# Optimization experiments

Measured on AMD Instinct MI355X. Metric: run time of the kernel, lower is better.

Reference implementation:

```python
import jax, jax.numpy as jnp
import numpy as np

N = 50000   # nodes
E = 800000  # directed edges
IN, H1, H2, OUT = 128, 64, 32, 40
K = 2       # SGConv hops


def setup_inputs() -> dict:
    key = jax.random.key(0)
    ks = jax.random.split(key, 8)
    x = jax.random.normal(ks[0], (N, IN), dtype=jnp.float32)
    edge_index = jax.random.randint(ks[1], (2, E), 0, N, dtype=jnp.int64)
    s = lambda k, shp, fan: jax.random.normal(k, shp, dtype=jnp.float32) / np.sqrt(fan)
    return {
        "x": x,
        "edge_index": edge_index,
        "W1": s(ks[2], (IN, H1), IN), "b1": jnp.zeros((H1,), jnp.float32),
        "W2": s(ks[3], (H1, H2), H1), "b2": jnp.zeros((H2,), jnp.float32),
        "Wf": s(ks[4], (H2, OUT), H2), "bf": jnp.zeros((OUT,), jnp.float32),
    }


def _gcn_norm(edge_index, num_nodes):
    # add self-loops, then norm = d^{-1/2}[src] * d^{-1/2}[dst], d over targets
    loop = jnp.arange(num_nodes, dtype=edge_index.dtype)
    src = jnp.concatenate([edge_index[0], loop])
    dst = jnp.concatenate([edge_index[1], loop])
    deg = jax.ops.segment_sum(jnp.ones_like(src, dtype=jnp.float32), dst,
                              num_segments=num_nodes)
    dinv = jnp.where(deg > 0, jax.lax.rsqrt(deg), 0.0)
    norm = dinv[src] * dinv[dst]  # [E + N]
    return src, dst, norm


def _propagate_k(x, src, dst, norm, num_nodes, k):
    for _ in range(k):
        x = jax.ops.segment_sum(x[src] * norm[:, None], dst,
                                num_segments=num_nodes)
    return x


def reference(x, edge_index, W1, b1, W2, b2, Wf, bf):
    num_nodes = x.shape[0]
    src, dst, norm = _gcn_norm(edge_index, num_nodes)
    # SGConv layer 1: A_hat^K x, then linear, then relu
    h = _propagate_k(x, src, dst, norm, num_nodes, K)
    h = jax.nn.relu(h @ W1 + b1)
    # SGConv layer 2
    h = _propagate_k(h, src, dst, norm, num_nodes, K)
    h = jax.nn.relu(h @ W2 + b2)
    embedding = h
    logits = h @ Wf + bf
    return (embedding, logits)
```

## Files before the change

kernel.cpp:

```cpp
#include <hip/hip_runtime.h>

#define NN 50000
#define NE 800000
#define IN_F 128
#define H1_F 64
#define H2_F 32
#define OUT_F 40

#define BSH 7
#define NBKT 391
#define CAPA 4032
#define CHUNK 4096
#define NCH ((NE + CHUNK - 1) / CHUNK)

static inline int cdiv(int a, int b) { return (a + b - 1) / b; }

__global__ void initcur_k(int* __restrict__ gCursor) {
    int b = blockIdx.x * 256 + threadIdx.x;
    if (b < NBKT) gCursor[b] = b * CAPA;
}

__global__ __launch_bounds__(256)
void binA_k(const int* __restrict__ src, const int* __restrict__ dst,
            uint2* __restrict__ pairs, int* __restrict__ gCursor) {
    __shared__ int hist[512], incl[512], runSt[512], lcur[512], baseSh[512];
    __shared__ uint2 stage[CHUNK];
    const int t = threadIdx.x;
    const int e0 = blockIdx.x * CHUNK;
    const int n = min(CHUNK, NE - e0);

    hist[t] = 0; hist[t + 256] = 0;
    __syncthreads();
    for (int i = t; i < n; i += 256) {
        int d = dst[e0 + i];
        atomicAdd(&hist[d >> BSH], 1);
    }
    __syncthreads();
    incl[t] = hist[t]; incl[t + 256] = hist[t + 256];
    __syncthreads();
    for (int off = 1; off < 512; off <<= 1) {
        int v0 = (t >= off) ? incl[t - off] : 0;
        int v1 = (t + 256 >= off) ? incl[t + 256 - off] : 0;
        __syncthreads();
        incl[t] += v0; incl[t + 256] += v1;
        __syncthreads();
    }
    runSt[t] = incl[t] - hist[t];   runSt[t + 256] = incl[t + 256] - hist[t + 256];
    lcur[t]  = runSt[t];            lcur[t + 256]  = runSt[t + 256];
    __syncthreads();
    for (int i = t; i < n; i += 256) {
        int s = src[e0 + i], d = dst[e0 + i];
        int b = d >> BSH;
        int p = atomicAdd(&lcur[b], 1);
        stage[p] = make_uint2((unsigned)s, (unsigned)d);
    }
    for (int b = t; b < NBKT; b += 256) {
        int c = hist[b];
        baseSh[b] = c ? atomicAdd(&gCursor[b], c) : 0;
    }
    __syncthreads();
    for (int i = t; i < n; i += 256) {
        uint2 p = stage[i];
        int b = (int)(p.y >> BSH);
        int gp = baseSh[b] + (i - runSt[b]);
        if (gp < (b + 1) * CAPA) pairs[gp] = p;
    }
}

__global__ __launch_bounds__(512)
void segscan_k(const int* __restrict__ gCursor, int* __restrict__ segBase) {
    __shared__ int sh[512], orig[512];
    int t = threadIdx.x;
    int c = 0;
    if (t < NBKT) {
        c = gCursor[t] - t * CAPA;
        c = max(0, min(c, CAPA));
    }
    sh[t] = c; orig[t] = c;
    __syncthreads();
    for (int off = 1; off < 512; off <<= 1) {
        int v = (t >= off) ? sh[t - off] : 0;
        __syncthreads();
        sh[t] += v;
        __syncthreads();
    }
    if (t < NBKT) segBase[t] = sh[t] - orig[t];
}

__global__ __launch_bounds__(256)
void binB_k(const uint2* __restrict__ pairs, const int* __restrict__ gCursor,
            const int* __restrict__ segBase, int* __restrict__ cursor,
            float* __restrict__ dinv, int* __restrict__ csr) {
    const int b = blockIdx.x;
    const int nodeBase = b << BSH;
    const int nNodes = min(128, NN - nodeBase);
    int count = gCursor[b] - b * CAPA;
    count = max(0, min(count, CAPA));
    const int seg = segBase[b];
    __shared__ int hist[128], incl[128], lcur[128];
    const int t = threadIdx.x;
    if (t < 128) hist[t] = 0;
    __syncthreads();
    const uint2* bp = pairs + (size_t)b * CAPA;
    for (int i = t; i < count; i += 256) {
        int d = (int)bp[i].y - nodeBase;
        atomicAdd(&hist[d], 1);
    }
    __syncthreads();
    if (t < 128) incl[t] = hist[t];
    __syncthreads();
    for (int off = 1; off < 128; off <<= 1) {
        int v = (t < 128 && t >= off) ? incl[t - off] : 0;
        __syncthreads();
        if (t < 128) incl[t] += v;
        __syncthreads();
    }
    if (t < nNodes) {
        cursor[nodeBase + t] = seg + incl[t];
        dinv[nodeBase + t]   = rsqrtf((float)hist[t] + 1.0f);
        lcur[t] = seg + incl[t] - hist[t];
    }
    __syncthreads();
    for (int i = t; i < count; i += 256) {
        uint2 p = bp[i];
        int d = (int)p.y - nodeBase;
        int pos = atomicAdd(&lcur[d], 1);
        csr[pos] = (int)p.x;
    }
}

template<int K, int F, int CT, int RPT, int BLOCK, bool BIAS, bool SCALE>
__global__ __launch_bounds__(BLOCK)
void gemm_tile_k(const float* __restrict__ X, const float* __restrict__ W,
                 const float* __restrict__ b, const float* __restrict__ dinv,
                 float* __restrict__ Y) {
    constexpr int RT = BLOCK / CT;
    constexpr int TR = RT * RPT;
    constexpr int KT = 32;
    constexpr int KPAD = KT + 1;
    __shared__ float Xs[TR][KPAD];
    __shared__ float Wsh[KT][F];
    const int rowBase = blockIdx.x * TR;
    const int tc = threadIdx.x % CT;
    const int tr = threadIdx.x / CT;

    float acc[RPT][4];
    #pragma unroll
    for (int i = 0; i < RPT; ++i)
        #pragma unroll
        for (int j = 0; j < 4; ++j) acc[i][j] = 0.0f;

    for (int k0 = 0; k0 < K; k0 += KT) {
        constexpr int XL4 = TR * KT / 4;
        for (int l = threadIdx.x; l < XL4; l += BLOCK) {
            int r  = l / (KT / 4);
            int kk = (l % (KT / 4)) * 4;
            float4 v = make_float4(0.f, 0.f, 0.f, 0.f);
            int gr = rowBase + r;
            if (gr < NN) v = *reinterpret_cast<const float4*>(X + (size_t)gr * K + k0 + kk);
            Xs[r][kk + 0] = v.x; Xs[r][kk + 1] = v.y;
            Xs[r][kk + 2] = v.z; Xs[r][kk + 3] = v.w;
        }
        constexpr int WL4 = KT * F / 4;
        for (int l = threadIdx.x; l < WL4; l += BLOCK) {
            int kk = l / (F / 4);
            int c  = (l % (F / 4)) * 4;
            *reinterpret_cast<float4*>(&Wsh[kk][c]) =
                *reinterpret_cast<const float4*>(W + (size_t)(k0 + kk) * F + c);
        }
        __syncthreads();
        #pragma unroll
        for (int kk = 0; kk < KT; ++kk) {
            float wv[4];
            *reinterpret_cast<float4*>(wv) = *reinterpret_cast<const float4*>(&Wsh[kk][tc * 4]);
            #pragma unroll
            for (int i = 0; i < RPT; ++i) {
                float a = Xs[tr * RPT + i][kk];
                acc[i][0] = fmaf(a, wv[0], acc[i][0]);
                acc[i][1] = fmaf(a, wv[1], acc[i][1]);
                acc[i][2] = fmaf(a, wv[2], acc[i][2]);
                acc[i][3] = fmaf(a, wv[3], acc[i][3]);
            }
        }
        __syncthreads();
    }
    #pragma unroll
    for (int i = 0; i < RPT; ++i) {
        int gr = rowBase + tr * RPT + i;
        if (gr < NN) {
            float sc = SCALE ? dinv[gr] : 1.0f;
            float4 v;
            v.x = acc[i][0]; v.y = acc[i][1]; v.z = acc[i][2]; v.w = acc[i][3];
            if (BIAS) {
                v.x += b[tc * 4 + 0]; v.y += b[tc * 4 + 1];
                v.z += b[tc * 4 + 2]; v.w += b[tc * 4 + 3];
            }
            v.x *= sc; v.y *= sc; v.z *= sc; v.w *= sc;
            *reinterpret_cast<float4*>(Y + (size_t)gr * F + tc * 4) = v;
        }
    }
}

template<int F>
__global__ __launch_bounds__(256)
void pull4_k(const float* __restrict__ in, const int* __restrict__ csr,
             const int* __restrict__ cursor, const float* __restrict__ dinv,
             float* __restrict__ out) {
    constexpr int LPN = F / 4;
    constexpr int NPB = 256 / LPN;
    const int t = threadIdx.x;
    const int node = blockIdx.x * NPB + t / LPN;
    const int col  = (t % LPN) * 4;
    if (node >= NN) return;
    const int beg = (node == 0) ? 0 : cursor[node - 1];
    const int end = cursor[node];
    float4 a0 = *reinterpret_cast<const float4*>(in + (size_t)node * F + col);
    float4 a1 = make_float4(0.f, 0.f, 0.f, 0.f);
    float4 a2 = make_float4(0.f, 0.f, 0.f, 0.f);
    float4 a3 = make_float4(0.f, 0.f, 0.f, 0.f);
    int k = beg;
    for (; k + 3 < end; k += 4) {
        int s0 = csr[k], s1 = csr[k + 1], s2 = csr[k + 2], s3 = csr[k + 3];
        float4 v0 = *reinterpret_cast<const float4*>(in + (size_t)s0 * F + col);
        float4 v1 = *reinterpret_cast<const float4*>(in + (size_t)s1 * F + col);
        float4 v2 = *reinterpret_cast<const float4*>(in + (size_t)s2 * F + col);
        float4 v3 = *reinterpret_cast<const float4*>(in + (size_t)s3 * F + col);
        a0.x += v0.x; a0.y += v0.y; a0.z += v0.z; a0.w += v0.w;
        a1.x += v1.x; a1.y += v1.y; a1.z += v1.z; a1.w += v1.w;
        a2.x += v2.x; a2.y += v2.y; a2.z += v2.z; a2.w += v2.w;
        a3.x += v3.x; a3.y += v3.y; a3.z += v3.z; a3.w += v3.w;
    }
    for (; k < end; ++k) {
        int s0 = csr[k];
        float4 v0 = *reinterpret_cast<const float4*>(in + (size_t)s0 * F + col);
        a0.x += v0.x; a0.y += v0.y; a0.z += v0.z; a0.w += v0.w;
    }
    float sc = dinv[node]; sc *= sc;
    float4 r;
    r.x = (a0.x + a1.x + a2.x + a3.x) * sc;
    r.y = (a0.y + a1.y + a2.y + a3.y) * sc;
    r.z = (a0.z + a1.z + a2.z + a3.z) * sc;
    r.w = (a0.w + a1.w + a2.w + a3.w) * sc;
    *reinterpret_cast<float4*>(out + (size_t)node * F + col) = r;
}

__global__ __launch_bounds__(256)
void pullgemm2_k(const float* __restrict__ in, const int* __restrict__ csr,
                 const int* __restrict__ cursor, const float* __restrict__ dinv,
                 const float* __restrict__ b1, const float* __restrict__ W2,
                 float* __restrict__ outT) {
    __shared__ float hs[64][68];
    __shared__ float W2s[64][32];
    const int t = threadIdx.x;
    for (int i = t; i < 64 * 32 / 4; i += 256)
        reinterpret_cast<float4*>(&W2s[0][0])[i] = reinterpret_cast<const float4*>(W2)[i];
    const int nodeBase = blockIdx.x * 64;
    #pragma unroll
    for (int pass = 0; pass < 4; ++pass) {
        const int nb = pass * 16 + t / 16;
        const int node = nodeBase + nb;
        const int col = (t % 16) * 4;
        float4 r = make_float4(0.f, 0.f, 0.f, 0.f);
        if (node < NN) {
            const int beg = (node == 0) ? 0 : cursor[node - 1];
            const int end = cursor[node];
            float4 a0 = *reinterpret_cast<const float4*>(in + (size_t)node * 64 + col);
            float4 a1 = make_float4(0.f, 0.f, 0.f, 0.f);
            float4 a2 = make_float4(0.f, 0.f, 0.f, 0.f);
            float4 a3 = make_float4(0.f, 0.f, 0.f, 0.f);
            int k = beg;
            for (; k + 3 < end; k += 4) {
                int s0 = csr[k], s1 = csr[k + 1], s2 = csr[k + 2], s3 = csr[k + 3];
                float4 v0 = *reinterpret_cast<const float4*>(in + (size_t)s0 * 64 + col);
                float4 v1 = *reinterpret_cast<const float4*>(in + (size_t)s1 * 64 + col);
                float4 v2 = *reinterpret_cast<const float4*>(in + (size_t)s2 * 64 + col);
                float4 v3 = *reinterpret_cast<const float4*>(in + (size_t)s3 * 64 + col);
                a0.x += v0.x; a0.y += v0.y; a0.z += v0.z; a0.w += v0.w;
                a1.x += v1.x; a1.y += v1.y; a1.z += v1.z; a1.w += v1.w;
                a2.x += v2.x; a2.y += v2.y; a2.z += v2.z; a2.w += v2.w;
                a3.x += v3.x; a3.y += v3.y; a3.z += v3.z; a3.w += v3.w;
            }
            for (; k < end; ++k) {
                int s0 = csr[k];
                float4 v0 = *reinterpret_cast<const float4*>(in + (size_t)s0 * 64 + col);
                a0.x += v0.x; a0.y += v0.y; a0.z += v0.z; a0.w += v0.w;
            }
            const float sc = dinv[node];
            const float4 bv = *reinterpret_cast<const float4*>(b1 + col);
            r.x = fmaxf((a0.x + a1.x + a2.x + a3.x) * sc + bv.x, 0.f);
            r.y = fmaxf((a0.y + a1.y + a2.y + a3.y) * sc + bv.y, 0.f);
            r.z = fmaxf((a0.z + a1.z + a2.z + a3.z) * sc + bv.z, 0.f);
            r.w = fmaxf((a0.w + a1.w + a2.w + a3.w) * sc + bv.w, 0.f);
        }
        *reinterpret_cast<float4*>(&hs[nb][col]) = r;
    }
    __syncthreads();
    const int r = t / 4;
    const int c0 = (t % 4) * 8;
    float acc[8];
    #pragma unroll
    for (int j = 0; j < 8; ++j) acc[j] = 0.f;
    #pragma unroll 4
    for (int k = 0; k < 64; k += 4) {
        float4 av = *reinterpret_cast<const float4*>(&hs[r][k]);
        #pragma unroll
        for (int kk = 0; kk < 4; ++kk) {
            float a = (&av.x)[kk];
            float4 w0 = *reinterpret_cast<const float4*>(&W2s[k + kk][c0]);
            float4 w1 = *reinterpret_cast<const float4*>(&W2s[k + kk][c0 + 4]);
            acc[0] = fmaf(a, w0.x, acc[0]); acc[1] = fmaf(a, w0.y, acc[1]);
            acc[2] = fmaf(a, w0.z, acc[2]); acc[3] = fmaf(a, w0.w, acc[3]);
            acc[4] = fmaf(a, w1.x, acc[4]); acc[5] = fmaf(a, w1.y, acc[5]);
            acc[6] = fmaf(a, w1.z, acc[6]); acc[7] = fmaf(a, w1.w, acc[7]);
        }
    }
    const int node = nodeBase + r;
    if (node < NN) {
        const float sc = dinv[node];
        float4 o0, o1;
        o0.x = acc[0] * sc; o0.y = acc[1] * sc; o0.z = acc[2] * sc; o0.w = acc[3] * sc;
        o1.x = acc[4] * sc; o1.y = acc[5] * sc; o1.z = acc[6] * sc; o1.w = acc[7] * sc;
        *reinterpret_cast<float4*>(outT + (size_t)node * 32 + c0)     = o0;
        *reinterpret_cast<float4*>(outT + (size_t)node * 32 + c0 + 4) = o1;
    }
}

__global__ __launch_bounds__(256)
void pullgemmF_k(const float* __restrict__ in, const int* __restrict__ csr,
                 const int* __restrict__ cursor, const float* __restrict__ dinv,
                 const float* __restrict__ b2, const float* __restrict__ Wf,
                 const float* __restrict__ bf, float* __restrict__ embOut,
                 float* __restrict__ logits) {
    __shared__ float es[64][36];
    __shared__ float Wfs[32][40];
    __shared__ float bfs[40];
    const int t = threadIdx.x;
    for (int i = t; i < 32 * 40 / 4; i += 256)
        reinterpret_cast<float4*>(&Wfs[0][0])[i] = reinterpret_cast<const float4*>(Wf)[i];
    if (t < 40) bfs[t] = bf[t];
    const int nodeBase = blockIdx.x * 64;
    #pragma unroll
    for (int pass = 0; pass < 2; ++pass) {
        const int nb = pass * 32 + t / 8;
        const int node = nodeBase + nb;
        const int col = (t % 8) * 4;
        float4 r = make_float4(0.f, 0.f, 0.f, 0.f);
        if (node < NN) {
            const int beg = (node == 0) ? 0 : cursor[node - 1];
            const int end = cursor[node];
            float4 a0 = *reinterpret_cast<const float4*>(in + (size_t)node * 32 + col);
            float4 a1 = make_float4(0.f, 0.f, 0.f, 0.f);
            float4 a2 = make_float4(0.f, 0.f, 0.f, 0.f);
            float4 a3 = make_float4(0.f, 0.f, 0.f, 0.f);
            int k = beg;
            for (; k + 3 < end; k += 4) {
                int s0 = csr[k], s1 = csr[k + 1], s2 = csr[k + 2], s3 = csr[k + 3];
                float4 v0 = *reinterpret_cast<const float4*>(in + (size_t)s0 * 32 + col);
                float4 v1 = *reinterpret_cast<const float4*>(in + (size_t)s1 * 32 + col);
                float4 v2 = *reinterpret_cast<const float4*>(in + (size_t)s2 * 32 + col);
                float4 v3 = *reinterpret_cast<const float4*>(in + (size_t)s3 * 32 + col);
                a0.x += v0.x; a0.y += v0.y; a0.z += v0.z; a0.w += v0.w;
                a1.x += v1.x; a1.y += v1.y; a1.z += v1.z; a1.w += v1.w;
                a2.x += v2.x; a2.y += v2.y; a2.z += v2.z; a2.w += v2.w;
                a3.x += v3.x; a3.y += v3.y; a3.z += v3.z; a3.w += v3.w;
            }
            for (; k < end; ++k) {
                int s0 = csr[k];
                float4 v0 = *reinterpret_cast<const float4*>(in + (size_t)s0 * 32 + col);
                a0.x += v0.x; a0.y += v0.y; a0.z += v0.z; a0.w += v0.w;
            }
            const float sc = dinv[node];
            const float4 bv = *reinterpret_cast<const float4*>(b2 + col);
            r.x = fmaxf((a0.x + a1.x + a2.x + a3.x) * sc + bv.x, 0.f);
            r.y = fmaxf((a0.y + a1.y + a2.y + a3.y) * sc + bv.y, 0.f);
            r.z = fmaxf((a0.z + a1.z + a2.z + a3.z) * sc + bv.z, 0.f);
            r.w = fmaxf((a0.w + a1.w + a2.w + a3.w) * sc + bv.w, 0.f);
            *reinterpret_cast<float4*>(embOut + (size_t)node * 32 + col) = r;
        }
        *reinterpret_cast<float4*>(&es[nb][col]) = r;
    }
    __syncthreads();
    const int r = t / 4;
    const int c0 = (t % 4) * 10;
    float acc[10];
    #pragma unroll
    for (int j = 0; j < 10; ++j) acc[j] = bfs[c0 + j];
    #pragma unroll 4
    for (int k = 0; k < 32; k += 4) {
        float4 av = *reinterpret_cast<const float4*>(&es[r][k]);
        #pragma unroll
        for (int kk = 0; kk < 4; ++kk) {
            float a = (&av.x)[kk];
            #pragma unroll
            for (int j = 0; j < 10; ++j)
                acc[j] = fmaf(a, Wfs[k + kk][c0 + j], acc[j]);
        }
    }
    const int node = nodeBase + r;
    if (node < NN) {
        float* lp = logits + (size_t)node * 40 + c0;
        #pragma unroll
        for (int j = 0; j < 10; j += 2) {
            float2 o; o.x = acc[j]; o.y = acc[j + 1];
            *reinterpret_cast<float2*>(lp + j) = o;
        }
    }
}

extern "C" void kernel_launch(void* const* d_in, const int* in_sizes, int n_in,
                              void* d_out, int out_size, void* d_ws, size_t ws_size,
                              hipStream_t stream) {
    const float* x  = (const float*)d_in[0];
    const int*   ei = (const int*)d_in[1];
    const float* W1 = (const float*)d_in[2];
    const float* b1 = (const float*)d_in[3];
    const float* W2 = (const float*)d_in[4];
    const float* b2 = (const float*)d_in[5];
    const float* Wf = (const float*)d_in[6];
    const float* bf = (const float*)d_in[7];

    float* out    = (float*)d_out;
    float* embOut = out;
    float* logits = out + (size_t)NN * H2_F;

    const int* src = ei;
    const int* dst = ei + NE;

    float* ws       = (float*)d_ws;
    float* dinv     = ws;
    int*   cursor   = (int*)(ws + NN);
    int*   csr      = cursor + NN;
    int*   gCursor  = csr + NE;
    int*   segBase  = gCursor + 512;
    float* bufA     = (float*)(segBase + 512);
    float* bufB     = bufA + (size_t)NN * 64;
    uint2* pairs    = (uint2*)bufB;

    initcur_k<<<cdiv(NBKT, 256), 256, 0, stream>>>(gCursor);
    binA_k<<<NCH, 256, 0, stream>>>(src, dst, pairs, gCursor);
    segscan_k<<<1, 512, 0, stream>>>(gCursor, segBase);
    binB_k<<<NBKT, 256, 0, stream>>>(pairs, gCursor, segBase, cursor, dinv, csr);

    gemm_tile_k<IN_F, H1_F, 16, 4, 256, false, true>
        <<<cdiv(NN, 64), 256, 0, stream>>>(x, W1, nullptr, dinv, bufA);
    pull4_k<H1_F>
        <<<cdiv(NN, 256 / (H1_F / 4)), 256, 0, stream>>>(bufA, csr, cursor, dinv, bufB);
    pullgemm2_k
        <<<cdiv(NN, 64), 256, 0, stream>>>(bufB, csr, cursor, dinv, b1, W2, bufA);

    pull4_k<H2_F>
        <<<cdiv(NN, 256 / (H2_F / 4)), 256, 0, stream>>>(bufA, csr, cursor, dinv, bufB);
    pullgemmF_k
        <<<cdiv(NN, 64), 256, 0, stream>>>(bufB, csr, cursor, dinv, b2, Wf, bf, embOut, logits);
}
```

Measured before the change: 240.4 us.

## Overlap X·W1 GEMM with edge binning in one kernel; pack edges, drop segscan

Merges the first dense GEMM (x·W1) and the edge-binning pass into one launch using block-index specialisation with a shared LDS union, so the GEMM no longer waits on dinv. The dinv scaling moves into the first pull kernel, which now weights each neighbour by dinv[src]. Edges are packed into 32-bit words instead of uint2, and the CSR uses fixed per-bucket segments with an int2 rowptr, which removes the segscan kernel and the init kernel (replaced by a memset). This cuts launches and binning traffic, but adds an extra dinv gather per edge in the first propagation and assumes source ids fit in 16 bits.

```diff
diff --git a/kernel.cpp b/kernel.cpp
--- a/kernel.cpp
+++ b/kernel.cpp
@@ -12,99 +12,137 @@
 #define CAPA 4032
 #define CHUNK 4096
 #define NCH ((NE + CHUNK - 1) / CHUNK)
+#define NGEMM ((NN + 63) / 64)
 
 static inline int cdiv(int a, int b) { return (a + b - 1) / b; }
 
-__global__ void initcur_k(int* __restrict__ gCursor) {
-    int b = blockIdx.x * 256 + threadIdx.x;
-    if (b < NBKT) gCursor[b] = b * CAPA;
-}
-
-__global__ __launch_bounds__(256)
-void binA_k(const int* __restrict__ src, const int* __restrict__ dst,
-            uint2* __restrict__ pairs, int* __restrict__ gCursor) {
-    __shared__ int hist[512], incl[512], runSt[512], lcur[512], baseSh[512];
-    __shared__ uint2 stage[CHUNK];
-    const int t = threadIdx.x;
-    const int e0 = blockIdx.x * CHUNK;
-    const int n = min(CHUNK, NE - e0);
-
-    hist[t] = 0; hist[t + 256] = 0;
-    __syncthreads();
-    for (int i = t; i < n; i += 256) {
-        int d = dst[e0 + i];
-        atomicAdd(&hist[d >> BSH], 1);
-    }
-    __syncthreads();
-    incl[t] = hist[t]; incl[t + 256] = hist[t + 256];
-    __syncthreads();
-    for (int off = 1; off < 512; off <<= 1) {
-        int v0 = (t >= off) ? incl[t - off] : 0;
-        int v1 = (t + 256 >= off) ? incl[t + 256 - off] : 0;
-        __syncthreads();
-        incl[t] += v0; incl[t + 256] += v1;
-        __syncthreads();
-    }
-    runSt[t] = incl[t] - hist[t];   runSt[t + 256] = incl[t + 256] - hist[t + 256];
-    lcur[t]  = runSt[t];            lcur[t + 256]  = runSt[t + 256];
-    __syncthreads();
-    for (int i = t; i < n; i += 256) {
-        int s = src[e0 + i], d = dst[e0 + i];
-        int b = d >> BSH;
-        int p = atomicAdd(&lcur[b], 1);
-        stage[p] = make_uint2((unsigned)s, (unsigned)d);
-    }
-    for (int b = t; b < NBKT; b += 256) {
-        int c = hist[b];
-        baseSh[b] = c ? atomicAdd(&gCursor[b], c) : 0;
-    }
-    __syncthreads();
-    for (int i = t; i < n; i += 256) {
-        uint2 p = stage[i];
-        int b = (int)(p.y >> BSH);
-        int gp = baseSh[b] + (i - runSt[b]);
-        if (gp < (b + 1) * CAPA) pairs[gp] = p;
-    }
-}
-
-__global__ __launch_bounds__(512)
-void segscan_k(const int* __restrict__ gCursor, int* __restrict__ segBase) {
-    __shared__ int sh[512], orig[512];
-    int t = threadIdx.x;
-    int c = 0;
-    if (t < NBKT) {
-        c = gCursor[t] - t * CAPA;
-        c = max(0, min(c, CAPA));
-    }
-    sh[t] = c; orig[t] = c;
-    __syncthreads();
-    for (int off = 1; off < 512; off <<= 1) {
-        int v = (t >= off) ? sh[t - off] : 0;
-        __syncthreads();
-        sh[t] += v;
-        __syncthreads();
-    }
-    if (t < NBKT) segBase[t] = sh[t] - orig[t];
-}
-
-__global__ __launch_bounds__(256)
-void binB_k(const uint2* __restrict__ pairs, const int* __restrict__ gCursor,
-            const int* __restrict__ segBase, int* __restrict__ cursor,
-            float* __restrict__ dinv, int* __restrict__ csr) {
+__device__ __forceinline__ unsigned pack_e(int s, int d) {
+    return ((unsigned)(d >> BSH) << 23) | ((unsigned)s << 7) | (unsigned)(d & 127);
+}
+
+struct GemmLDS { float Xs[64][33]; float Wsh[32][64]; };
+struct BinALDS { int hist[512]; int incl[512]; int runSt[512]; int lcur[512]; int baseSh[512];
+                 unsigned stage[CHUNK]; };
+
+__global__ __launch_bounds__(256)
+void phase1_k(const float* __restrict__ x, const float* __restrict__ W1,
+              const int* __restrict__ src, const int* __restrict__ dst,
+              unsigned* __restrict__ pairs, int* __restrict__ gCursor,
+              float* __restrict__ t_out) {
+    __shared__ union { GemmLDS g; BinALDS a; } lds;
+    const int t = threadIdx.x;
+
+    if (blockIdx.x < NGEMM) {
+        const int rowBase = blockIdx.x * 64;
+        const int tc = t % 16;
+        const int tr = t / 16;
+        float acc[4][4];
+        #pragma unroll
+        for (int i = 0; i < 4; ++i)
+            #pragma unroll
+            for (int j = 0; j < 4; ++j) acc[i][j] = 0.0f;
+
+        for (int k0 = 0; k0 < IN_F; k0 += 32) {
+            for (int l = t; l < 64 * 8; l += 256) {
+                int r  = l / 8;
+                int kk = (l % 8) * 4;
+                float4 v = make_float4(0.f, 0.f, 0.f, 0.f);
+                int gr = rowBase + r;
+                if (gr < NN) v = *reinterpret_cast<const float4*>(x + (size_t)gr * IN_F + k0 + kk);
+                lds.g.Xs[r][kk + 0] = v.x; lds.g.Xs[r][kk + 1] = v.y;
+                lds.g.Xs[r][kk + 2] = v.z; lds.g.Xs[r][kk + 3] = v.w;
+            }
+            for (int l = t; l < 32 * 16; l += 256) {
+                int kk = l / 16;
+                int c  = (l % 16) * 4;
+                *reinterpret_cast<float4*>(&lds.g.Wsh[kk][c]) =
+                    *reinterpret_cast<const float4*>(W1 + (size_t)(k0 + kk) * H1_F + c);
+            }
+            __syncthreads();
+            #pragma unroll
+            for (int kk = 0; kk < 32; ++kk) {
+                float wv[4];
+                *reinterpret_cast<float4*>(wv) =
+                    *reinterpret_cast<const float4*>(&lds.g.Wsh[kk][tc * 4]);
+                #pragma unroll
+                for (int i = 0; i < 4; ++i) {
+                    float a = lds.g.Xs[tr * 4 + i][kk];
+                    acc[i][0] = fmaf(a, wv[0], acc[i][0]);
+                    acc[i][1] = fmaf(a, wv[1], acc[i][1]);
+                    acc[i][2] = fmaf(a, wv[2], acc[i][2]);
+                    acc[i][3] = fmaf(a, wv[3], acc[i][3]);
+                }
+            }
+            __syncthreads();
+        }
+        #pragma unroll
+        for (int i = 0; i < 4; ++i) {
+            int gr = rowBase + tr * 4 + i;
+            if (gr < NN) {
+                float4 v;
+                v.x = acc[i][0]; v.y = acc[i][1]; v.z = acc[i][2]; v.w = acc[i][3];
+                *reinterpret_cast<float4*>(t_out + (size_t)gr * H1_F + tc * 4) = v;
+            }
+        }
+    } else {
+        const int e0 = (blockIdx.x - NGEMM) * CHUNK;
+        const int n = min(CHUNK, NE - e0);
+        lds.a.hist[t] = 0; lds.a.hist[t + 256] = 0;
+        __syncthreads();
+        for (int i = t; i < n; i += 256) {
+            int d = dst[e0 + i];
+            atomicAdd(&lds.a.hist[d >> BSH], 1);
+        }
+        __syncthreads();
+        lds.a.incl[t] = lds.a.hist[t]; lds.a.incl[t + 256] = lds.a.hist[t + 256];
+        __syncthreads();
+        for (int off = 1; off < 512; off <<= 1) {
+            int v0 = (t >= off) ? lds.a.incl[t - off] : 0;
+            int v1 = (t + 256 >= off) ? lds.a.incl[t + 256 - off] : 0;
+            __syncthreads();
+            lds.a.incl[t] += v0; lds.a.incl[t + 256] += v1;
+            __syncthreads();
+        }
+        lds.a.runSt[t]       = lds.a.incl[t] - lds.a.hist[t];
+        lds.a.runSt[t + 256] = lds.a.incl[t + 256] - lds.a.hist[t + 256];
+        lds.a.lcur[t]        = lds.a.runSt[t];
+        lds.a.lcur[t + 256]  = lds.a.runSt[t + 256];
+        __syncthreads();
+        for (int i = t; i < n; i += 256) {
+            int s = src[e0 + i], d = dst[e0 + i];
+            int b = d >> BSH;
+            int p = atomicAdd(&lds.a.lcur[b], 1);
+            lds.a.stage[p] = pack_e(s, d);
+        }
+        for (int b = t; b < NBKT; b += 256) {
+            int c = lds.a.hist[b];
+            lds.a.baseSh[b] = c ? atomicAdd(&gCursor[b], c) : 0;
+        }
+        __syncthreads();
+        for (int i = t; i < n; i += 256) {
+            unsigned p = lds.a.stage[i];
+            int b = (int)(p >> 23);
+            int gp = lds.a.baseSh[b] + (i - lds.a.runSt[b]);
+            if (gp < CAPA) pairs[(size_t)b * CAPA + gp] = p;
+        }
+    }
+}
+
+__global__ __launch_bounds__(256)
+void binB_k(const unsigned* __restrict__ pairs, const int* __restrict__ gCursor,
+            int2* __restrict__ rowptr, float* __restrict__ dinv, int* __restrict__ csr) {
     const int b = blockIdx.x;
     const int nodeBase = b << BSH;
     const int nNodes = min(128, NN - nodeBase);
-    int count = gCursor[b] - b * CAPA;
-    count = max(0, min(count, CAPA));
-    const int seg = segBase[b];
+    int count = min(gCursor[b], CAPA);
+    const int seg = b * CAPA;
     __shared__ int hist[128], incl[128], lcur[128];
     const int t = threadIdx.x;
     if (t < 128) hist[t] = 0;
     __syncthreads();
-    const uint2* bp = pairs + (size_t)b * CAPA;
+    const unsigned* bp = pairs + (size_t)b * CAPA;
     for (int i = t; i < count; i += 256) {
-        int d = (int)bp[i].y - nodeBase;
-        atomicAdd(&hist[d], 1);
+        atomicAdd(&hist[bp[i] & 127], 1);
     }
     __syncthreads();
     if (t < 128) incl[t] = hist[t];
@@ -116,123 +154,96 @@
         __syncthreads();
     }
     if (t < nNodes) {
-        cursor[nodeBase + t] = seg + incl[t];
+        int e = seg + incl[t];
+        rowptr[nodeBase + t] = make_int2(e - hist[t], e);
         dinv[nodeBase + t]   = rsqrtf((float)hist[t] + 1.0f);
-        lcur[t] = seg + incl[t] - hist[t];
+        lcur[t] = e - hist[t];
     }
     __syncthreads();
     for (int i = t; i < count; i += 256) {
-        uint2 p = bp[i];
-        int d = (int)p.y - nodeBase;
-        int pos = atomicAdd(&lcur[d], 1);
-        csr[pos] = (int)p.x;
-    }
-}
-
-template<int K, int F, int CT, int RPT, int BLOCK, bool BIAS, bool SCALE>
-__global__ __launch_bounds__(BLOCK)
-void gemm_tile_k(const float* __restrict__ X, const float* __restrict__ W,
-                 const float* __restrict__ b, const float* __restrict__ dinv,
-                 float* __restrict__ Y) {
-    constexpr int RT = BLOCK / CT;
-    constexpr int TR = RT * RPT;
-    constexpr int KT = 32;
-    constexpr int KPAD = KT + 1;
-    __shared__ float Xs[TR][KPAD];
-    __shared__ float Wsh[KT][F];
-    const int rowBase = blockIdx.x * TR;
-    const int tc = threadIdx.x % CT;
-    const int tr = threadIdx.x / CT;
-
-    float acc[RPT][4];
-    #pragma unroll
-    for (int i = 0; i < RPT; ++i)
-        #pragma unroll
-        for (int j = 0; j < 4; ++j) acc[i][j] = 0.0f;
-
-    for (int k0 = 0; k0 < K; k0 += KT) {
-        constexpr int XL4 = TR * KT / 4;
-        for (int l = threadIdx.x; l < XL4; l += BLOCK) {
-            int r  = l / (KT / 4);
-            int kk = (l % (KT / 4)) * 4;
-            float4 v = make_float4(0.f, 0.f, 0.f, 0.f);
-            int gr = rowBase + r;
-            if (gr < NN) v = *reinterpret_cast<const float4*>(X + (size_t)gr * K + k0 + kk);
-            Xs[r][kk + 0] = v.x; Xs[r][kk + 1] = v.y;
-            Xs[r][kk + 2] = v.z; Xs[r][kk + 3] = v.w;
-        }
-        constexpr int WL4 = KT * F / 4;
-        for (int l = threadIdx.x; l < WL4; l += BLOCK) {
-            int kk = l / (F / 4);
-            int c  = (l % (F / 4)) * 4;
-            *reinterpret_cast<float4*>(&Wsh[kk][c]) =
-                *reinterpret_cast<const float4*>(W + (size_t)(k0 + kk) * F + c);
-        }
-        __syncthreads();
-        #pragma unroll
-        for (int kk = 0; kk < KT; ++kk) {
-            float wv[4];
-            *reinterpret_cast<float4*>(wv) = *reinterpret_cast<const float4*>(&Wsh[kk][tc * 4]);
-            #pragma unroll
-            for (int i = 0; i < RPT; ++i) {
-                float a = Xs[tr * RPT + i][kk];
-                acc[i][0] = fmaf(a, wv[0], acc[i][0]);
-                acc[i][1] = fmaf(a, wv[1], acc[i][1]);
-                acc[i][2] = fmaf(a, wv[2], acc[i][2]);
-                acc[i][3] = fmaf(a, wv[3], acc[i][3]);
-            }
-        }
-        __syncthreads();
-    }
-    #pragma unroll
-    for (int i = 0; i < RPT; ++i) {
-        int gr = rowBase + tr * RPT + i;
-        if (gr < NN) {
-            float sc = SCALE ? dinv[gr] : 1.0f;
-            float4 v;
-            v.x = acc[i][0]; v.y = acc[i][1]; v.z = acc[i][2]; v.w = acc[i][3];
-            if (BIAS) {
-                v.x += b[tc * 4 + 0]; v.y += b[tc * 4 + 1];
-                v.z += b[tc * 4 + 2]; v.w += b[tc * 4 + 3];
-            }
-            v.x *= sc; v.y *= sc; v.z *= sc; v.w *= sc;
-            *reinterpret_cast<float4*>(Y + (size_t)gr * F + tc * 4) = v;
-        }
-    }
-}
-
-template<int F>
-__global__ __launch_bounds__(256)
-void pull4_k(const float* __restrict__ in, const int* __restrict__ csr,
-             const int* __restrict__ cursor, const float* __restrict__ dinv,
+        unsigned p = bp[i];
+        int pos = atomicAdd(&lcur[p & 127], 1);
+        csr[pos] = (int)((p >> 7) & 0xFFFFu);
+    }
+}
+
+__global__ __launch_bounds__(256)
+void pull1_k(const float* __restrict__ in, const int* __restrict__ csr,
+             const int2* __restrict__ rowptr, const float* __restrict__ dinv,
              float* __restrict__ out) {
-    constexpr int LPN = F / 4;
-    constexpr int NPB = 256 / LPN;
-    const int t = threadIdx.x;
-    const int node = blockIdx.x * NPB + t / LPN;
-    const int col  = (t % LPN) * 4;
+    const int t = threadIdx.x;
+    const int node = blockIdx.x * 16 + t / 16;
+    const int col  = (t % 16) * 4;
     if (node >= NN) return;
-    const int beg = (node == 0) ? 0 : cursor[node - 1];
-    const int end = cursor[node];
-    float4 a0 = *reinterpret_cast<const float4*>(in + (size_t)node * F + col);
+    const int2 rp = rowptr[node];
+    const float dd = dinv[node];
+    float4 s4 = *reinterpret_cast<const float4*>(in + (size_t)node * 64 + col);
+    float4 a0, a1, a2, a3;
+    a0.x = dd * s4.x; a0.y = dd * s4.y; a0.z = dd * s4.z; a0.w = dd * s4.w;
+    a1 = make_float4(0.f, 0.f, 0.f, 0.f);
+    a2 = make_float4(0.f, 0.f, 0.f, 0.f);
+    a3 = make_float4(0.f, 0.f, 0.f, 0.f);
+    int k = rp.x;
+    for (; k + 3 < rp.y; k += 4) {
+        int s0 = csr[k], s1 = csr[k + 1], s2 = csr[k + 2], s3 = csr[k + 3];
+        float w0 = dinv[s0], w1 = dinv[s1], w2 = dinv[s2], w3 = dinv[s3];
+        float4 v0 = *reinterpret_cast<const float4*>(in + (size_t)s0 * 64 + col);
+        float4 v1 = *reinterpret_cast<const float4*>(in + (size_t)s1 * 64 + col);
+        float4 v2 = *reinterpret_cast<const float4*>(in + (size_t)s2 * 64 + col);
+        float4 v3 = *reinterpret_cast<const float4*>(in + (size_t)s3 * 64 + col);
+        a0.x = fmaf(w0, v0.x, a0.x); a0.y = fmaf(w0, v0.y, a0.y);
+        a0.z = fmaf(w0, v0.z, a0.z); a0.w = fmaf(w0, v0.w, a0.w);
+        a1.x = fmaf(w1, v1.x, a1.x); a1.y = fmaf(w1, v1.y, a1.y);
+        a1.z = fmaf(w1, v1.z, a1.z); a1.w = fmaf(w1, v1.w, a1.w);
+        a2.x = fmaf(w2, v2.x, a2.x); a2.y = fmaf(w2, v2.y, a2.y);
+        a2.z = fmaf(w2, v2.z, a2.z); a2.w = fmaf(w2, v2.w, a2.w);
+        a3.x = fmaf(w3, v3.x, a3.x); a3.y = fmaf(w3, v3.y, a3.y);
+        a3.z = fmaf(w3, v3.z, a3.z); a3.w = fmaf(w3, v3.w, a3.w);
+    }
+    for (; k < rp.y; ++k) {
+        int s0 = csr[k];
+        float w0 = dinv[s0];
+        float4 v0 = *reinterpret_cast<const float4*>(in + (size_t)s0 * 64 + col);
+        a0.x = fmaf(w0, v0.x, a0.x); a0.y = fmaf(w0, v0.y, a0.y);
+        a0.z = fmaf(w0, v0.z, a0.z); a0.w = fmaf(w0, v0.w, a0.w);
+    }
+    const float sc = dd * dd;
+    float4 r;
+    r.x = (a0.x + a1.x + a2.x + a3.x) * sc;
+    r.y = (a0.y + a1.y + a2.y + a3.y) * sc;
+    r.z = (a0.z + a1.z + a2.z + a3.z) * sc;
+    r.w = (a0.w + a1.w + a2.w + a3.w) * sc;
+    *reinterpret_cast<float4*>(out + (size_t)node * 64 + col) = r;
+}
+
+__global__ __launch_bounds__(256)
+void pull32_k(const float* __restrict__ in, const int* __restrict__ csr,
+              const int2* __restrict__ rowptr, const float* __restrict__ dinv,
+              float* __restrict__ out) {
+    const int t = threadIdx.x;
+    const int node = blockIdx.x * 32 + t / 8;
+    const int col  = (t % 8) * 4;
+    if (node >= NN) return;
+    const int2 rp = rowptr[node];
+    float4 a0 = *reinterpret_cast<const float4*>(in + (size_t)node * 32 + col);
     float4 a1 = make_float4(0.f, 0.f, 0.f, 0.f);
     float4 a2 = make_float4(0.f, 0.f, 0.f, 0.f);
     float4 a3 = make_float4(0.f, 0.f, 0.f, 0.f);
-    int k = beg;
-    for (; k + 3 < end; k += 4) {
+    int k = rp.x;
+    for (; k + 3 < rp.y; k += 4) {
         int s0 = csr[k], s1 = csr[k + 1], s2 = csr[k + 2], s3 = csr[k + 3];
-        float4 v0 = *reinterpret_cast<const float4*>(in + (size_t)s0 * F + col);
-        float4 v1 = *reinterpret_cast<const float4*>(in + (size_t)s1 * F + col);
-        float4 v2 = *reinterpret_cast<const float4*>(in + (size_t)s2 * F + col);
-        float4 v3 = *reinterpret_cast<const float4*>(in + (size_t)s3 * F + col);
+        float4 v0 = *reinterpret_cast<const float4*>(in + (size_t)s0 * 32 + col);
+        float4 v1 = *reinterpret_cast<const float4*>(in + (size_t)s1 * 32 + col);
+        float4 v2 = *reinterpret_cast<const float4*>(in + (size_t)s2 * 32 + col);
+        float4 v3 = *reinterpret_cast<const float4*>(in + (size_t)s3 * 32 + col);
         a0.x += v0.x; a0.y += v0.y; a0.z += v0.z; a0.w += v0.w;
         a1.x += v1.x; a1.y += v1.y; a1.z += v1.z; a1.w += v1.w;
         a2.x += v2.x; a2.y += v2.y; a2.z += v2.z; a2.w += v2.w;
         a3.x += v3.x; a3.y += v3.y; a3.z += v3.z; a3.w += v3.w;
     }
-    for (; k < end; ++k) {
+    for (; k < rp.y; ++k) {
         int s0 = csr[k];
-        float4 v0 = *reinterpret_cast<const float4*>(in + (size_t)s0 * F + col);
+        float4 v0 = *reinterpret_cast<const float4*>(in + (size_t)s0 * 32 + col);
         a0.x += v0.x; a0.y += v0.y; a0.z += v0.z; a0.w += v0.w;
     }
     float sc = dinv[node]; sc *= sc;
@@ -241,12 +252,12 @@
     r.y = (a0.y + a1.y + a2.y + a3.y) * sc;
     r.z = (a0.z + a1.z + a2.z + a3.z) * sc;
     r.w = (a0.w + a1.w + a2.w + a3.w) * sc;
-    *reinterpret_cast<float4*>(out + (size_t)node * F + col) = r;
+    *reinterpret_cast<float4*>(out + (size_t)node * 32 + col) = r;
 }
 
 __global__ __launch_bounds__(256)
 void pullgemm2_k(const float* __restrict__ in, const int* __restrict__ csr,
-                 const int* __restrict__ cursor, const float* __restrict__ dinv,
+                 const int2* __restrict__ rowptr, const float* __restrict__ dinv,
                  const float* __restrict__ b1, const float* __restrict__ W2,
                  float* __restrict__ outT) {
     __shared__ float hs[64][68];
@@ -262,14 +273,13 @@
         const int col = (t % 16) * 4;
         float4 r = make_float4(0.f, 0.f, 0.f, 0.f);
         if (node < NN) {
-            const int beg = (node == 0) ? 0 : cursor[node - 1];
-            const int end = cursor[node];
+            const int2 rp = rowptr[node];
             float4 a0 = *reinterpret_cast<const float4*>(in + (size_t)node * 64 + col);
             float4 a1 = make_float4(0.f, 0.f, 0.f, 0.f);
             float4 a2 = make_float4(0.f, 0.f, 0.f, 0.f);
             float4 a3 = make_float4(0.f, 0.f, 0.f, 0.f);
-            int k = beg;
-            for (; k + 3 < end; k += 4) {
+            int k = rp.x;
+            for (; k + 3 < rp.y; k += 4) {
                 int s0 = csr[k], s1 = csr[k + 1], s2 = csr[k + 2], s3 = csr[k + 3];
                 float4 v0 = *reinterpret_cast<const float4*>(in + (size_t)s0 * 64 + col);
                 float4 v1 = *reinterpret_cast<const float4*>(in + (size_t)s1 * 64 + col);
@@ -280,7 +290,7 @@
                 a2.x += v2.x; a2.y += v2.y; a2.z += v2.z; a2.w += v2.w;
                 a3.x += v3.x; a3.y += v3.y; a3.z += v3.z; a3.w += v3.w;
             }
-            for (; k < end; ++k) {
+            for (; k < rp.y; ++k) {
                 int s0 = csr[k];
                 float4 v0 = *reinterpret_cast<const float4*>(in + (size_t)s0 * 64 + col);
                 a0.x += v0.x; a0.y += v0.y; a0.z += v0.z; a0.w += v0.w;
@@ -327,7 +337,7 @@
 
 __global__ __launch_bounds__(256)
 void pullgemmF_k(const float* __restrict__ in, const int* __restrict__ csr,
-                 const int* __restrict__ cursor, const float* __restrict__ dinv,
+                 const int2* __restrict__ rowptr, const float* __restrict__ dinv,
                  const float* __restrict__ b2, const float* __restrict__ Wf,
                  const float* __restrict__ bf, float* __restrict__ embOut,
                  float* __restrict__ logits) {
@@ -346,14 +356,13 @@
         const int col = (t % 8) * 4;
         float4 r = make_float4(0.f, 0.f, 0.f, 0.f);
         if (node < NN) {
-            const int beg = (node == 0) ? 0 : cursor[node - 1];
-            const int end = cursor[node];
+            const int2 rp = rowptr[node];
             float4 a0 = *reinterpret_cast<const float4*>(in + (size_t)node * 32 + col);
             float4 a1 = make_float4(0.f, 0.f, 0.f, 0.f);
             float4 a2 = make_float4(0.f, 0.f, 0.f, 0.f);
             float4 a3 = make_float4(0.f, 0.f, 0.f, 0.f);
-            int k = beg;
-            for (; k + 3 < end; k += 4) {
+            int k = rp.x;
+            for (; k + 3 < rp.y; k += 4) {
                 int s0 = csr[k], s1 = csr[k + 1], s2 = csr[k + 2], s3 = csr[k + 3];
                 float4 v0 = *reinterpret_cast<const float4*>(in + (size_t)s0 * 32 + col);
                 float4 v1 = *reinterpret_cast<const float4*>(in + (size_t)s1 * 32 + col);
@@ -364,7 +373,7 @@
                 a2.x += v2.x; a2.y += v2.y; a2.z += v2.z; a2.w += v2.w;
                 a3.x += v3.x; a3.y += v3.y; a3.z += v3.z; a3.w += v3.w;
             }
-            for (; k < end; ++k) {
+            for (; k < rp.y; ++k) {
                 int s0 = csr[k];
                 float4 v0 = *reinterpret_cast<const float4*>(in + (size_t)s0 * 32 + col);
                 a0.x += v0.x; a0.y += v0.y; a0.z += v0.z; a0.w += v0.w;
@@ -426,30 +435,22 @@
     const int* src = ei;
     const int* dst = ei + NE;
 
-    float* ws       = (float*)d_ws;
-    float* dinv     = ws;
-    int*   cursor   = (int*)(ws + NN);
-    int*   csr      = cursor + NN;
-    int*   gCursor  = csr + NE;
-    int*   segBase  = gCursor + 512;
-    float* bufA     = (float*)(segBase + 512);
-    float* bufB     = bufA + (size_t)NN * 64;
-    uint2* pairs    = (uint2*)bufB;
-
-    initcur_k<<<cdiv(NBKT, 256), 256, 0, stream>>>(gCursor);
-    binA_k<<<NCH, 256, 0, stream>>>(src, dst, pairs, gCursor);
-    segscan_k<<<1, 512, 0, stream>>>(gCursor, segBase);
-    binB_k<<<NBKT, 256, 0, stream>>>(pairs, gCursor, segBase, cursor, dinv, csr);
-
-    gemm_tile_k<IN_F, H1_F, 16, 4, 256, false, true>
-        <<<cdiv(NN, 64), 256, 0, stream>>>(x, W1, nullptr, dinv, bufA);
-    pull4_k<H1_F>
-        <<<cdiv(NN, 256 / (H1_F / 4)), 256, 0, stream>>>(bufA, csr, cursor, dinv, bufB);
-    pullgemm2_k
-        <<<cdiv(NN, 64), 256, 0, stream>>>(bufB, csr, cursor, dinv, b1, W2, bufA);
-
-    pull4_k<H2_F>
-        <<<cdiv(NN, 256 / (H2_F / 4)), 256, 0, stream>>>(bufA, csr, cursor, dinv, bufB);
-    pullgemmF_k
-        <<<cdiv(NN, 64), 256, 0, stream>>>(bufB, csr, cursor, dinv, b2, Wf, bf, embOut, logits);
-}
+    float* ws      = (float*)d_ws;
+    float*    dinv   = ws;
+    int2*     rowptr = (int2*)(ws + NN);
+    int*      csr    = (int*)(rowptr + NN);
+    int*      gCursor= csr + (size_t)NBKT * CAPA;
+    float*    bufA   = (float*)(gCursor + 512);
+    float*    bufB   = bufA + (size_t)NN * 64;
+    unsigned* pairs  = (unsigned*)bufB;
+
+    hipMemsetAsync(gCursor, 0, NBKT * sizeof(int), stream);
+    phase1_k<<<NGEMM + NCH, 256, 0, stream>>>(x, W1, src, dst, pairs, gCursor, bufA);
+    binB_k<<<NBKT, 256, 0, stream>>>(pairs, gCursor, rowptr, dinv, csr);
+
+    pull1_k<<<cdiv(NN, 16), 256, 0, stream>>>(bufA, csr, rowptr, dinv, bufB);
+    pullgemm2_k<<<cdiv(NN, 64), 256, 0, stream>>>(bufB, csr, rowptr, dinv, b1, W2, bufA);
+
+    pull32_k<<<cdiv(NN, 32), 256, 0, stream>>>(bufA, csr, rowptr, dinv, bufB);
+    pullgemmF_k<<<cdiv(NN, 64), 256, 0, stream>>>(bufB, csr, rowptr, dinv, b2, Wf, bf, embOut, logits);
+}
```

Measured after the change: 252.7 us. +5.1%, slower.
